# Kernel optimization log

Hardware: AMD Instinct MI355X
Metric: run time of the kernel (lower is better)

The kernel has to match this reference:

```python
import jax, jax.numpy as jnp
import numpy as np

# FlowNetC correlation config: kernel_size=1, so no kernel-window averaging;
# pad_size == max_displacement -> output spatial size == input spatial size.
B, C, H, W = 8, 256, 48, 64
MAX_DISP = 20   # max_displacement
STRIDE2 = 2     # displacement stride
PAD = 20        # pad_size
GRID_RAD = MAX_DISP // STRIDE2            # 10
GRID_W = 2 * GRID_RAD + 1                 # 21 -> 441 displacement channels


def setup_inputs() -> dict:
    key = jax.random.key(0)
    k1, k2 = jax.random.split(key)
    return {
        "input1": jax.random.normal(k1, (B, C, H, W), dtype=jnp.float32),
        "input2": jax.random.normal(k2, (B, C, H, W), dtype=jnp.float32),
    }


def _correlation(input1, input2):
    b, c, h, w = input1.shape
    p2 = jnp.pad(input2, ((0, 0), (0, 0), (PAD, PAD), (PAD, PAD)))
    # Displacement start offsets into the padded map. dy-major ordering matches
    # the CUDA kernel: top_channel = dy_idx * GRID_W + dx_idx.
    d = np.arange(-GRID_RAD, GRID_RAD + 1) * STRIDE2 + PAD  # [21]
    offs = np.stack(np.meshgrid(d, d, indexing="ij"), axis=-1).reshape(-1, 2)
    offs = jnp.asarray(offs, dtype=jnp.int32)  # [441, 2] (dy, dx)
    sumelems = jnp.float32(c)  # kernel_size^2 * C with kernel_size=1

    def step(carry, o):
        shifted = jax.lax.dynamic_slice(p2, (0, 0, o[0], o[1]), (b, c, h, w))
        # mean over channels of elementwise product -> [B, H, W]
        return carry, jnp.sum(input1 * shifted, axis=1) / sumelems

    _, ys = jax.lax.scan(step, 0, offs)          # [441, B, H, W]
    return jnp.transpose(ys, (1, 0, 2, 3))       # [B, 441, H, W]


def reference(input1, input2):
    return _correlation(input1, input2)
```

## Files before the change

kernel.cpp:

```cpp
#include <hip/hip_runtime.h>

typedef __bf16 bf16x8 __attribute__((ext_vector_type(8)));
typedef float f32x4 __attribute__((ext_vector_type(4)));
typedef float f32x16 __attribute__((ext_vector_type(16)));

#define CC 256
#define HH 48
#define WW 64
#define HW (HH * WW)
#define NB 8
#define GW 21

__global__ __launch_bounds__(256) void prep_kernel(const float* __restrict__ in1,
                                                   const float* __restrict__ in2,
                                                   unsigned short* __restrict__ o1,
                                                   unsigned short* __restrict__ o2)
{
    __shared__ float lds[CC * 33];
    int blk  = blockIdx.x;
    int sel  = (blk >= 768);
    int blk2 = sel ? blk - 768 : blk;
    int b  = blk2 & 7;
    int st = blk2 >> 3;
    int s0 = st * 32;
    const float* src = sel ? in2 : in1;
    unsigned short* dst = sel ? o2 : o1;
    float scale = sel ? 1.0f : (1.0f / 256.0f);

    int t = threadIdx.x;
    int sidx  = t & 31;
    int cbase = t >> 5;
    const float* sb = src + (size_t)b * CC * HW + s0;
    #pragma unroll
    for (int p = 0; p < 32; ++p) {
        int c = cbase + p * 8;
        lds[c * 33 + sidx] = sb[(size_t)c * HW + sidx] * scale;
    }
    __syncthreads();

    int y  = s0 >> 6;
    int xb = s0 & 63;
    int s  = t & 31;
    int c8 = t >> 5;
    unsigned short* db = dst + (size_t)(b * HH + y) * 32 * 64 * 8;
    int x = xb + s;
    int xoff = (x & 1) * 32 + (x >> 1);
    #pragma unroll
    for (int it = 0; it < 4; ++it) {
        int cblk = it * 8 + c8;
        unsigned dw[4];
        #pragma unroll
        for (int d = 0; d < 4; ++d) {
            unsigned u0 = __builtin_bit_cast(unsigned, lds[(cblk * 8 + 2 * d) * 33 + s]);
            u0 += 0x7fffu + ((u0 >> 16) & 1u);
            unsigned u1 = __builtin_bit_cast(unsigned, lds[(cblk * 8 + 2 * d + 1) * 33 + s]);
            u1 += 0x7fffu + ((u1 >> 16) & 1u);
            dw[d] = (u0 >> 16) | (u1 & 0xffff0000u);
        }
        *(uint4*)(db + ((size_t)cblk * 64 + xoff) * 8) =
            make_uint4(dw[0], dw[1], dw[2], dw[3]);
    }
}

__global__ __launch_bounds__(256, 2) void corr_kernel(const unsigned short* __restrict__ in1F,
                                                      const unsigned short* __restrict__ in2F,
                                                      float* __restrict__ out)
{
    __shared__ float dts[4][2304];

    int blk = blockIdx.x;
    int b   = blk & 7;
    int r   = blk >> 3;
    int yi  = r / 3;
    int t   = r - yi * 3;
    int ys0 = yi - 20;
    int ys1 = ys0 + 2;

    int tid  = threadIdx.x;
    int w    = tid >> 6;
    int lane = tid & 63;
    int q    = 4 * t + w;
    int yo   = ys0 + 20 - 4 * q;

    if (q > 10 || yo < 0 || yo >= HH) return;

    bool vs_[2];
    vs_[0] = (ys0 >= 0) && (ys0 < HH);
    vs_[1] = (ys1 >= 0) && (ys1 < HH);
    int j0 = 2 * q;

    int l31 = lane & 31;
    int q2  = lane >> 5;
    int lofs = q2 * 512 + l31 * 8;

    const unsigned short* ar = in1F + (size_t)(b * HH + yo) * 16384 + lofs;
    const unsigned short* br_[2];
    br_[0] = in2F + (size_t)(b * HH + (vs_[0] ? ys0 : 0)) * 16384 + lofs;
    br_[1] = in2F + (size_t)(b * HH + (vs_[1] ? ys1 : 0)) * 16384 + lofs;

    bf16x8 Ab[4][2], Bb[4][2][2];
    #pragma unroll
    for (int s = 0; s < 3; ++s) {
        #pragma unroll
        for (int p = 0; p < 2; ++p)
            Ab[s][p] = *(const bf16x8*)(ar + s * 1024 + p * 256);
        #pragma unroll
        for (int jj = 0; jj < 2; ++jj)
            if (vs_[jj])
                #pragma unroll
                for (int p = 0; p < 2; ++p)
                    Bb[s][jj][p] = *(const bf16x8*)(br_[jj] + s * 1024 + p * 256);
    }

    f32x16 acc[2][2];
    #pragma unroll
    for (int jj = 0; jj < 2; ++jj)
        #pragma unroll
        for (int p = 0; p < 2; ++p)
            acc[jj][p] = (f32x16)(0.0f);

    #pragma unroll
    for (int kk = 0; kk < 16; ++kk) {
        if (kk < 13) {
            #pragma unroll
            for (int p = 0; p < 2; ++p)
                Ab[(kk + 3) & 3][p] =
                    *(const bf16x8*)(ar + (size_t)(kk + 3) * 1024 + p * 256);
            #pragma unroll
            for (int jj = 0; jj < 2; ++jj)
                if (vs_[jj])
                    #pragma unroll
                    for (int p = 0; p < 2; ++p)
                        Bb[(kk + 3) & 3][jj][p] =
                            *(const bf16x8*)(br_[jj] + (size_t)(kk + 3) * 1024 + p * 256);
        }
        #pragma unroll
        for (int jj = 0; jj < 2; ++jj)
            if (vs_[jj])
                #pragma unroll
                for (int p = 0; p < 2; ++p)
                    acc[jj][p] = __builtin_amdgcn_mfma_f32_32x32x16_bf16(
                        Ab[kk & 3][p], Bb[kk & 3][jj][p], acc[jj][p], 0, 0, 0);
    }

    float* dtw = dts[w];
    int xe = lane >> 1;
    int pe = lane & 1;
    #pragma unroll
    for (int jj = 0; jj < 2; ++jj) {
        int j = j0 + jj;
        if (j > 20) continue;
        float* orow = out + (((size_t)(b * 441 + j * GW)) * HH + yo) * WW;
        #pragma unroll
        for (int p = 0; p < 2; ++p)
            #pragma unroll
            for (int rq = 0; rq < 4; ++rq) {
                f32x4 v = { acc[jj][p][4 * rq], acc[jj][p][4 * rq + 1],
                            acc[jj][p][4 * rq + 2], acc[jj][p][4 * rq + 3] };
                *(f32x4*)(dtw + (size_t)(p * 32 + l31) * 36 + rq * 8 + q2 * 4) = v;
            }
        #pragma unroll
        for (int jx = 0; jx < GW; ++jx) {
            int ce = xe + jx - 10;
            float val = (ce >= 0 && ce < 32)
                      ? dtw[(size_t)(pe * 32 + ce) * 36 + xe] : 0.0f;
            __builtin_nontemporal_store(val, orow + (size_t)jx * HW + lane);
        }
    }
}

extern "C" void kernel_launch(void* const* d_in, const int* in_sizes, int n_in,
                              void* d_out, int out_size, void* d_ws, size_t ws_size,
                              hipStream_t stream)
{
    (void)in_sizes; (void)n_in; (void)out_size; (void)ws_size;
    const float* in1 = (const float*)d_in[0];
    const float* in2 = (const float*)d_in[1];
    float* out = (float*)d_out;

    unsigned short* in1F = (unsigned short*)d_ws;
    unsigned short* in2F = in1F + (size_t)NB * HW * CC;

    prep_kernel<<<dim3(1536), dim3(256), 0, stream>>>(in1, in2, in1F, in2F);
    corr_kernel<<<dim3(NB * 88 * 3), dim3(256), 0, stream>>>(in1F, in2F, out);
}
```

Baseline: 114.4 us.

## Remap correlation blocks to dy×8-row tiles and stage outputs in LDS

Result: slower. 120.7 us (+5.5%).

```diff
diff --git a/kernel.cpp b/kernel.cpp
--- a/kernel.cpp
+++ b/kernel.cpp
@@ -67,105 +67,93 @@
                                                       float* __restrict__ out)
 {
     __shared__ float dts[4][2304];
+    __shared__ float stage[GW * 8 * WW];
 
     int blk = blockIdx.x;
     int b   = blk & 7;
     int r   = blk >> 3;
-    int yi  = r / 3;
-    int t   = r - yi * 3;
-    int ys0 = yi - 20;
-    int ys1 = ys0 + 2;
+    int dy  = r % GW;
+    int yb  = r / GW;
+    int soff = 2 * dy - 20;
 
     int tid  = threadIdx.x;
     int w    = tid >> 6;
     int lane = tid & 63;
-    int q    = 4 * t + w;
-    int yo   = ys0 + 20 - 4 * q;
-
-    if (q > 10 || yo < 0 || yo >= HH) return;
-
-    bool vs_[2];
-    vs_[0] = (ys0 >= 0) && (ys0 < HH);
-    vs_[1] = (ys1 >= 0) && (ys1 < HH);
-    int j0 = 2 * q;
-
-    int l31 = lane & 31;
-    int q2  = lane >> 5;
+    int l31  = lane & 31;
+    int q2   = lane >> 5;
     int lofs = q2 * 512 + l31 * 8;
-
-    const unsigned short* ar = in1F + (size_t)(b * HH + yo) * 16384 + lofs;
-    const unsigned short* br_[2];
-    br_[0] = in2F + (size_t)(b * HH + (vs_[0] ? ys0 : 0)) * 16384 + lofs;
-    br_[1] = in2F + (size_t)(b * HH + (vs_[1] ? ys1 : 0)) * 16384 + lofs;
-
-    bf16x8 Ab[4][2], Bb[4][2][2];
-    #pragma unroll
-    for (int s = 0; s < 3; ++s) {
-        #pragma unroll
-        for (int p = 0; p < 2; ++p)
-            Ab[s][p] = *(const bf16x8*)(ar + s * 1024 + p * 256);
-        #pragma unroll
-        for (int jj = 0; jj < 2; ++jj)
-            if (vs_[jj])
-                #pragma unroll
-                for (int p = 0; p < 2; ++p)
-                    Bb[s][jj][p] = *(const bf16x8*)(br_[jj] + s * 1024 + p * 256);
-    }
-
-    f32x16 acc[2][2];
-    #pragma unroll
-    for (int jj = 0; jj < 2; ++jj)
-        #pragma unroll
-        for (int p = 0; p < 2; ++p)
-            acc[jj][p] = (f32x16)(0.0f);
-
-    #pragma unroll
-    for (int kk = 0; kk < 16; ++kk) {
-        if (kk < 13) {
-            #pragma unroll
-            for (int p = 0; p < 2; ++p)
-                Ab[(kk + 3) & 3][p] =
-                    *(const bf16x8*)(ar + (size_t)(kk + 3) * 1024 + p * 256);
-            #pragma unroll
-            for (int jj = 0; jj < 2; ++jj)
-                if (vs_[jj])
-                    #pragma unroll
-                    for (int p = 0; p < 2; ++p)
-                        Bb[(kk + 3) & 3][jj][p] =
-                            *(const bf16x8*)(br_[jj] + (size_t)(kk + 3) * 1024 + p * 256);
-        }
-        #pragma unroll
-        for (int jj = 0; jj < 2; ++jj)
-            if (vs_[jj])
-                #pragma unroll
-                for (int p = 0; p < 2; ++p)
-                    acc[jj][p] = __builtin_amdgcn_mfma_f32_32x32x16_bf16(
-                        Ab[kk & 3][p], Bb[kk & 3][jj][p], acc[jj][p], 0, 0, 0);
-    }
 
     float* dtw = dts[w];
     int xe = lane >> 1;
     int pe = lane & 1;
-    #pragma unroll
-    for (int jj = 0; jj < 2; ++jj) {
-        int j = j0 + jj;
-        if (j > 20) continue;
-        float* orow = out + (((size_t)(b * 441 + j * GW)) * HH + yo) * WW;
+
+    #pragma unroll 1
+    for (int i = 0; i < 2; ++i) {
+        int yloc = 2 * w + i;
+        int yo   = 8 * yb + yloc;
+        int ys   = yo + soff;
+        bool vs  = (ys >= 0) && (ys < HH);
+
+        f32x16 acc[2];
+        acc[0] = (f32x16)(0.0f);
+        acc[1] = (f32x16)(0.0f);
+
+        if (vs) {
+            const unsigned short* ar = in1F + (size_t)(b * HH + yo) * 16384 + lofs;
+            const unsigned short* br = in2F + (size_t)(b * HH + ys) * 16384 + lofs;
+
+            bf16x8 Ab[4][2], Bb[4][2];
+            #pragma unroll
+            for (int s = 0; s < 3; ++s)
+                #pragma unroll
+                for (int p = 0; p < 2; ++p) {
+                    Ab[s][p] = *(const bf16x8*)(ar + (size_t)s * 1024 + p * 256);
+                    Bb[s][p] = *(const bf16x8*)(br + (size_t)s * 1024 + p * 256);
+                }
+
+            #pragma unroll
+            for (int kk = 0; kk < 16; ++kk) {
+                if (kk < 13) {
+                    #pragma unroll
+                    for (int p = 0; p < 2; ++p) {
+                        Ab[(kk + 3) & 3][p] =
+                            *(const bf16x8*)(ar + (size_t)(kk + 3) * 1024 + p * 256);
+                        Bb[(kk + 3) & 3][p] =
+                            *(const bf16x8*)(br + (size_t)(kk + 3) * 1024 + p * 256);
+                    }
+                }
+                #pragma unroll
+                for (int p = 0; p < 2; ++p)
+                    acc[p] = __builtin_amdgcn_mfma_f32_32x32x16_bf16(
+                        Ab[kk & 3][p], Bb[kk & 3][p], acc[p], 0, 0, 0);
+            }
+        }
+
         #pragma unroll
         for (int p = 0; p < 2; ++p)
             #pragma unroll
             for (int rq = 0; rq < 4; ++rq) {
-                f32x4 v = { acc[jj][p][4 * rq], acc[jj][p][4 * rq + 1],
-                            acc[jj][p][4 * rq + 2], acc[jj][p][4 * rq + 3] };
+                f32x4 v = { acc[p][4 * rq], acc[p][4 * rq + 1],
+                            acc[p][4 * rq + 2], acc[p][4 * rq + 3] };
                 *(f32x4*)(dtw + (size_t)(p * 32 + l31) * 36 + rq * 8 + q2 * 4) = v;
             }
         #pragma unroll
         for (int jx = 0; jx < GW; ++jx) {
             int ce = xe + jx - 10;
-            float val = (ce >= 0 && ce < 32)
+            float val = (vs && ce >= 0 && ce < 32)
                       ? dtw[(size_t)(pe * 32 + ce) * 36 + xe] : 0.0f;
-            __builtin_nontemporal_store(val, orow + (size_t)jx * HW + lane);
+            stage[jx * 512 + yloc * 64 + lane] = val;
         }
+    }
+
+    __syncthreads();
+
+    size_t obase = ((size_t)(b * 441 + dy * GW) * HH + yb * 8) * WW;
+    for (int s = tid; s < GW * 128; s += 256) {
+        int dxi = s >> 7;
+        int rem = s & 127;
+        f32x4 v = *(const f32x4*)(stage + dxi * 512 + rem * 4);
+        __builtin_nontemporal_store(v, (f32x4*)(out + obase + (size_t)dxi * HW + rem * 4));
     }
 }
 
@@ -182,5 +170,5 @@
     unsigned short* in2F = in1F + (size_t)NB * HW * CC;
 
     prep_kernel<<<dim3(1536), dim3(256), 0, stream>>>(in1, in2, in1F, in2F);
-    corr_kernel<<<dim3(NB * 88 * 3), dim3(256), 0, stream>>>(in1F, in2F, out);
+    corr_kernel<<<dim3(NB * GW * 6), dim3(256), 0, stream>>>(in1F, in2F, out);
 }
```
